# Kernel optimization log

Measured on AMD Instinct MI355X. Metric: run time of the kernel, lower is better.

Reference implementation:

```python
import jax, jax.numpy as jnp
import numpy as np

RADIUS = 2.0  # ball-query radius (float forward arg in the original; fixed here)


def _conv1x1(x, W, b):
    # 1x1 Conv2D over NHWC == per-point linear layer
    return jnp.einsum('bmsc,cd->bmsd', x, W) + b


def _ball_query(xyz, new_xyz, radius, nsample):
    """For each cluster center, take the first (by index) nsample points within
    radius, padding with the first found neighbor (TF ball-query semantics).
    xyz: (B,N,3), new_xyz: (B,M,3) -> idx (B,M,nsample) int32."""
    N = xyz.shape[1]
    d2 = jnp.sum((new_xyz[:, :, None, :] - xyz[:, None, :, :]) ** 2, axis=-1)  # (B,M,N)
    valid = d2 < radius * radius
    key = jnp.where(valid, jnp.arange(N, dtype=jnp.int32)[None, None, :], N)
    order = jnp.argsort(key, axis=-1)[..., :nsample]          # (B,M,nsample)
    skey = jnp.take_along_axis(key, order, axis=-1)
    idx = jnp.where(skey < N, order, order[..., :1])          # pad with first neighbor
    return idx


def setup_inputs() -> dict:
    key = jax.random.key(0)
    ks = jax.random.split(key, 8)
    B, N = 8, 8192
    xyz = jax.random.normal(ks[0], (B, N, 3), dtype=jnp.float32)

    def w(k, cin, cout):
        return (jax.random.normal(k, (cin, cout), dtype=jnp.float32) / np.sqrt(cin)).astype(jnp.float32)

    z = lambda c: jnp.zeros((c,), jnp.float32)
    inp = {
        'xyz': xyz,
        'W1': w(ks[1], 3, 64),    'b1': z(64),
        'W2': w(ks[2], 64, 128),  'b2': z(128),
        'W3': w(ks[3], 128, 256), 'b3': z(256),
        'W4': w(ks[4], 256, 128), 'b4': z(128),
        'W5': w(ks[5], 128, 64),  'b5': z(64),
        'Wa': w(ks[6], 64, 1),    'ba': z(1),
        'Wo': w(ks[7], 64, 2),    'bo': z(2),
        'num_clusters': 512,
        'num_samples': 64,
    }
    return inp


def reference(xyz, W1, b1, W2, b2, W3, b3, W4, b4, W5, b5, Wa, ba, Wo, bo,
              num_clusters, num_samples):
    # sample cluster centers (deterministic stand-in for random subsampling)
    new_xyz = xyz[:, :num_clusters]                                    # (B,M,3)
    idx = _ball_query(xyz, new_xyz, RADIUS, num_samples)               # (B,M,S)
    grouped = jax.vmap(lambda pts, i: pts[i])(xyz, idx)                # (B,M,S,3)
    g = (grouped - new_xyz[:, :, None, :]) / RADIUS                    # normalize_radius

    # shared per-point MLP (1x1 convs, relu)
    h = jax.nn.relu(_conv1x1(g, W1, b1))
    h = jax.nn.relu(_conv1x1(h, W2, b2))
    h = jax.nn.relu(_conv1x1(h, W3, b3))
    # MaxPoolAxis: max over samples, keepdims
    h = jnp.max(h, axis=2, keepdims=True)                              # (B,M,1,256)
    # mlp2 convs (linear, no activation in source)
    h = _conv1x1(h, W4, b4)
    h = _conv1x1(h, W5, b5)                                            # (B,M,1,64)

    attention = jax.nn.softplus(_conv1x1(h, Wa, ba))[:, :, 0, 0]       # (B,M)
    o = _conv1x1(h, Wo, bo)[:, :, 0, :]                                # (B,M,2)
    o = o / jnp.sqrt(jnp.maximum(jnp.sum(o * o, axis=-1, keepdims=True), 1e-8))
    orientation = jnp.arctan2(o[..., 1], o[..., 0])                    # (B,M)
    return new_xyz, idx, attention, orientation
```

## Files before the change

kernel.cpp:

```cpp
#include <hip/hip_runtime.h>
#include <math.h>

#define BB 8
#define NN 8192
#define MM 512
#define SS 64
#define NCLUST (BB*MM)

#define OUT_IDX   (BB*MM*3)
#define OUT_ATT   (OUT_IDX + BB*MM*SS)
#define OUT_ORI   (OUT_ATT + BB*MM)

#define WS_W3 8192

typedef short v8s __attribute__((ext_vector_type(8)));
typedef float v4f __attribute__((ext_vector_type(4)));

static __device__ __forceinline__ unsigned short f2bf(float x) {
    unsigned int u = __float_as_uint(x);
    u += 0x7FFFu + ((u >> 16) & 1u);
    return (unsigned short)(u >> 16);
}

__global__ void pack_weights(const float* __restrict__ W2,
                             const float* __restrict__ W3,
                             unsigned short* __restrict__ ws)
{
    const int gid = blockIdx.x * 256 + threadIdx.x;
    const float* W; unsigned short* dst; int N, kt, nt, lane;
    if (gid < 1024) {
        W = W2; N = 128;
        const int tile = gid >> 6; lane = gid & 63;
        kt = tile >> 3; nt = tile & 7;
        dst = ws + (size_t)(tile * 64 + lane) * 8;
    } else {
        const int g = gid - 1024;
        W = W3; N = 256;
        const int tile = g >> 6; lane = g & 63;
        kt = tile >> 4; nt = tile & 15;
        dst = ws + WS_W3 + (size_t)(tile * 64 + lane) * 8;
    }
    const int k0 = kt * 32 + (lane >> 4) * 8;
    const int n  = nt * 16 + (lane & 15);
    union { unsigned short u[8]; v8s v; } f;
    #pragma unroll
    for (int j = 0; j < 8; ++j) f.u[j] = f2bf(W[(k0 + j) * N + n]);
    *(v8s*)dst = f.v;
}

__global__ __launch_bounds__(256, 4) void feat3d_fused(
    const float* __restrict__ xyz,
    const float* __restrict__ W1, const float* __restrict__ b1,
    const float* __restrict__ b2, const float* __restrict__ b3,
    const unsigned short* __restrict__ Wp,
    const float* __restrict__ W4, const float* __restrict__ b4,
    const float* __restrict__ W5, const float* __restrict__ b5,
    const float* __restrict__ Wa, const float* __restrict__ ba,
    const float* __restrict__ Wo, const float* __restrict__ bo,
    float* __restrict__ out)
{
    __shared__ __align__(16) unsigned char lds[24576];
    unsigned short* a2p = (unsigned short*)lds;
    unsigned short* a3p = (unsigned short*)(lds + 8192);
    int*   ws_idx = (int*)(lds + 8192);
    float* ws_g   = (float*)(lds + 9216);
    int*   ls_cnt = (int*)(lds + 12288);
    float* ls_w1  = (float*)(lds + 12304);
    float* ls_g   = (float*)(lds + 13328);

    float* vbuf   = (float*)lds;
    float* h4part = (float*)(lds + 1024);
    float* h4f    = (float*)(lds + 5120);
    float* h5p    = (float*)(lds + 5632);

    const int t   = threadIdx.x;
    const int wv  = t >> 6;
    const int l   = t & 63;
    const int q   = l >> 4;
    const int r16 = l & 15;
    const int blk = blockIdx.x;
    const int b   = blk >> 9;
    const int m   = blk & 511;
    const float* xb = xyz + (size_t)b * (NN * 3);

    const v8s* W2f = (const v8s*)Wp;
    v8s bfr[2][2];
    #pragma unroll
    for (int kt = 0; kt < 2; ++kt)
        #pragma unroll
        for (int ni = 0; ni < 2; ++ni)
            bfr[kt][ni] = W2f[(kt*8 + 2*wv + ni)*64 + l];

    const float cx = xb[m*3+0], cy = xb[m*3+1], cz = xb[m*3+2];

    if (t < 3) out[(b*MM + m)*3 + t] = xb[m*3 + t];

    if (t < 64) {
        ls_w1[t*4+0] = W1[t];
        ls_w1[t*4+1] = W1[64 + t];
        ls_w1[t*4+2] = W1[128 + t];
        ls_w1[t*4+3] = b1[t];
    }

    {
        const int base = wv * 2048;
        int cntw = 0;
        for (int it = 0; it < 32 && cntw < SS; ++it) {
            const int j = base + it*64 + l;
            const float dx = xb[j*3+0] - cx;
            const float dy = xb[j*3+1] - cy;
            const float dz = xb[j*3+2] - cz;
            const float d2 = __fadd_rn(__fadd_rn(__fmul_rn(dx,dx), __fmul_rn(dy,dy)),
                                       __fmul_rn(dz,dz));
            const bool valid = d2 < 4.0f;
            const unsigned long long mask = __ballot(valid);
            const int below = __popcll(mask & ((1ull << l) - 1ull));
            const int pos = cntw + below;
            if (valid && pos < SS) {
                ws_idx[wv*64 + pos]      = j;
                ws_g[(wv*64 + pos)*3 + 0] = dx * 0.5f;
                ws_g[(wv*64 + pos)*3 + 1] = dy * 0.5f;
                ws_g[(wv*64 + pos)*3 + 2] = dz * 0.5f;
            }
            cntw += (int)__popcll(mask);
        }
        if (l == 0) ls_cnt[wv] = (cntw < SS) ? cntw : SS;
    }
    __syncthreads();

    if (t < SS) {
        const int c0 = ls_cnt[0], c1 = ls_cnt[1], c2 = ls_cnt[2], c3 = ls_cnt[3];
        int s, off;
        if (t < c0 + c1 + c2 + c3) {
            if (t < c0)                 { s = 0; off = t; }
            else if (t < c0 + c1)       { s = 1; off = t - c0; }
            else if (t < c0 + c1 + c2)  { s = 2; off = t - c0 - c1; }
            else                        { s = 3; off = t - c0 - c1 - c2; }
        } else {
            s = (c0 > 0) ? 0 : (c1 > 0) ? 1 : (c2 > 0) ? 2 : 3;
            off = 0;
        }
        const int e = s*64 + off;
        out[OUT_IDX + (b*MM + m)*SS + t] = (float)ws_idx[e];
        ls_g[t*4+0] = ws_g[e*3+0];
        ls_g[t*4+1] = ws_g[e*3+1];
        ls_g[t*4+2] = ws_g[e*3+2];
    }
    __syncthreads();

    {
        const int s = wv*16 + r16;
        const float4 g4 = *(const float4*)&ls_g[s*4];
        #pragma unroll
        for (int kt = 0; kt < 2; ++kt) {
            union { unsigned short u[8]; v8s v; } fr;
            #pragma unroll
            for (int j = 0; j < 8; ++j) {
                const int c = kt*32 + q*8 + j;
                const float4 w = *(const float4*)&ls_w1[c*4];
                const float h = fmaf(g4.x, w.x, fmaf(g4.y, w.y, fmaf(g4.z, w.z, w.w)));
                fr.u[j] = f2bf(fmaxf(h, 0.f));
            }
            *(v8s*)&a2p[((kt*4 + wv)*64 + l)*8] = fr.v;
        }
    }
    __syncthreads();

    {
        const v4f z = {0.f, 0.f, 0.f, 0.f};
        v4f acc[4][2];
        #pragma unroll
        for (int mt = 0; mt < 4; ++mt) { acc[mt][0] = z; acc[mt][1] = z; }

        #pragma unroll
        for (int kt = 0; kt < 2; ++kt)
            #pragma unroll
            for (int mt = 0; mt < 4; ++mt) {
                const v8s a = *(const v8s*)&a2p[((kt*4 + mt)*64 + l)*8];
                #pragma unroll
                for (int ni = 0; ni < 2; ++ni)
                    acc[mt][ni] = __builtin_amdgcn_mfma_f32_16x16x32_bf16(
                        a, bfr[kt][ni], acc[mt][ni], 0, 0, 0);
            }

        #pragma unroll
        for (int ni = 0; ni < 2; ++ni) {
            const int c2  = (2*wv + ni)*16 + r16;
            const float bias = b2[c2];
            const int kt3 = c2 >> 5;
            const int lhi = ((c2 >> 3) & 3) << 4;
            const int j3  = c2 & 7;
            #pragma unroll
            for (int mt = 0; mt < 4; ++mt)
                #pragma unroll
                for (int rg = 0; rg < 4; ++rg) {
                    const float h = fmaxf(acc[mt][ni][rg] + bias, 0.f);
                    const int s15 = q*4 + rg;
                    a3p[((kt3*4 + mt)*64 + (lhi | s15))*8 + j3] = f2bf(h);
                }
        }
    }
    __syncthreads();

    {
        const v8s* W3f = (const v8s*)(Wp + WS_W3);

        #pragma unroll
        for (int np = 0; np < 2; ++np) {
            const int nt0 = 4*wv + 2*np;
            const v4f z = {0.f, 0.f, 0.f, 0.f};
            v4f acc[4][2];
            #pragma unroll
            for (int mt = 0; mt < 4; ++mt) { acc[mt][0] = z; acc[mt][1] = z; }

            v8s bb0 = W3f[(0*16 + nt0    )*64 + l];
            v8s bb1 = W3f[(0*16 + nt0 + 1)*64 + l];
            #pragma unroll
            for (int kt = 0; kt < 4; ++kt) {
                v8s a[4];
                #pragma unroll
                for (int mt = 0; mt < 4; ++mt)
                    a[mt] = *(const v8s*)&a3p[((kt*4 + mt)*64 + l)*8];
                v8s nb0, nb1;
                if (kt < 3) {
                    nb0 = W3f[((kt+1)*16 + nt0    )*64 + l];
                    nb1 = W3f[((kt+1)*16 + nt0 + 1)*64 + l];
                }
                #pragma unroll
                for (int mt = 0; mt < 4; ++mt) {
                    acc[mt][0] = __builtin_amdgcn_mfma_f32_16x16x32_bf16(
                        a[mt], bb0, acc[mt][0], 0, 0, 0);
                    acc[mt][1] = __builtin_amdgcn_mfma_f32_16x16x32_bf16(
                        a[mt], bb1, acc[mt][1], 0, 0, 0);
                }
                if (kt < 3) { bb0 = nb0; bb1 = nb1; }
            }

            #pragma unroll
            for (int ni = 0; ni < 2; ++ni) {
                float mx = acc[0][ni][0];
                #pragma unroll
                for (int mt = 0; mt < 4; ++mt)
                    #pragma unroll
                    for (int rg = 0; rg < 4; ++rg)
                        mx = fmaxf(mx, acc[mt][ni][rg]);
                mx = fmaxf(mx, __shfl_xor(mx, 16));
                mx = fmaxf(mx, __shfl_xor(mx, 32));
                if (q == 0) {
                    const int c = (nt0 + ni)*16 + r16;
                    vbuf[c] = fmaxf(mx + b3[c], 0.f);
                }
            }
        }
    }
    __syncthreads();

    {
        const int cgp = t & 31;
        const int kp  = t >> 5;
        const float4* W4v = (const float4*)W4;
        const float4* vb4 = (const float4*)&vbuf[kp*32];
        float4 acc = make_float4(0.f, 0.f, 0.f, 0.f);
        #pragma unroll
        for (int kk4 = 0; kk4 < 8; ++kk4) {
            const float4 vv = vb4[kk4];
            const int k = kp*32 + kk4*4;
            const float4 w0 = W4v[(k+0)*32 + cgp];
            const float4 w1 = W4v[(k+1)*32 + cgp];
            const float4 w2 = W4v[(k+2)*32 + cgp];
            const float4 w3 = W4v[(k+3)*32 + cgp];
            acc.x = fmaf(vv.x, w0.x, fmaf(vv.y, w1.x, fmaf(vv.z, w2.x, fmaf(vv.w, w3.x, acc.x))));
            acc.y = fmaf(vv.x, w0.y, fmaf(vv.y, w1.y, fmaf(vv.z, w2.y, fmaf(vv.w, w3.y, acc.y))));
            acc.z = fmaf(vv.x, w0.z, fmaf(vv.y, w1.z, fmaf(vv.z, w2.z, fmaf(vv.w, w3.z, acc.z))));
            acc.w = fmaf(vv.x, w0.w, fmaf(vv.y, w1.w, fmaf(vv.z, w2.w, fmaf(vv.w, w3.w, acc.w))));
        }
        *(float4*)&h4part[kp*128 + cgp*4] = acc;
    }
    __syncthreads();
    if (t < 128) {
        float s = b4[t];
        #pragma unroll
        for (int kp = 0; kp < 8; ++kp) s += h4part[kp*128 + t];
        h4f[t] = s;
    }
    __syncthreads();

    {
        const int c5 = t & 63;
        const int kq = t >> 6;
        const float* W5c = W5 + c5;
        float acc = 0.f;
        for (int k = kq*32; k < kq*32 + 32; k += 4) {
            const float4 hh = *(const float4*)&h4f[k];
            acc = fmaf(hh.x, W5c[(k+0)*64],
                  fmaf(hh.y, W5c[(k+1)*64],
                  fmaf(hh.z, W5c[(k+2)*64],
                  fmaf(hh.w, W5c[(k+3)*64], acc))));
        }
        h5p[t] = acc;
    }
    __syncthreads();

    if (t < 64) {
        const float h5v = h5p[t] + h5p[64 + t] + h5p[128 + t] + h5p[192 + t] + b5[t];
        float va = h5v * Wa[t];
        float v0 = h5v * Wo[2*t + 0];
        float v1 = h5v * Wo[2*t + 1];
        #pragma unroll
        for (int off = 32; off > 0; off >>= 1) {
            va += __shfl_down(va, off);
            v0 += __shfl_down(v0, off);
            v1 += __shfl_down(v1, off);
        }
        if (t == 0) {
            const float a = va + ba[0];
            out[OUT_ATT + blk] = fmaxf(a, 0.f) + log1pf(expf(-fabsf(a)));
            out[OUT_ORI + blk] = atan2f(v1 + bo[1], v0 + bo[0]);
        }
    }
}

extern "C" void kernel_launch(void* const* d_in, const int* in_sizes, int n_in,
                              void* d_out, int out_size, void* d_ws, size_t ws_size,
                              hipStream_t stream) {
    const float* xyz = (const float*)d_in[0];
    const float* W1  = (const float*)d_in[1];
    const float* b1  = (const float*)d_in[2];
    const float* W2  = (const float*)d_in[3];
    const float* b2  = (const float*)d_in[4];
    const float* W3  = (const float*)d_in[5];
    const float* b3  = (const float*)d_in[6];
    const float* W4  = (const float*)d_in[7];
    const float* b4  = (const float*)d_in[8];
    const float* W5  = (const float*)d_in[9];
    const float* b5  = (const float*)d_in[10];
    const float* Wa  = (const float*)d_in[11];
    const float* ba  = (const float*)d_in[12];
    const float* Wo  = (const float*)d_in[13];
    const float* bo  = (const float*)d_in[14];

    unsigned short* ws = (unsigned short*)d_ws;

    pack_weights<<<dim3(20), dim3(256), 0, stream>>>(W2, W3, ws);
    feat3d_fused<<<dim3(NCLUST), dim3(256), 0, stream>>>(
        xyz, W1, b1, b2, b3, ws, W4, b4, W5, b5, Wa, ba, Wo, bo, (float*)d_out);
}
```

Before: 142.2 us.

## Process two clusters per 512-thread block with block-wide ordered ball query scan

Each block now handles two cluster centers with 512 threads, four waves per cluster. The ball query no longer gives each wave a fixed 2048-point slice. Instead it scans 256 points per step in order across four waves, shares ballot masks through LDS with a barrier each step, and stops once both clusters have 64 neighbors. This removes the over-scan of each wave's whole slice and amortizes weight loads across two clusters. The cost is a __syncthreads per 256 points, doubled LDS, and wave divergence when one cluster finishes early.

```diff
diff --git a/kernel.cpp b/kernel.cpp
--- a/kernel.cpp
+++ b/kernel.cpp
@@ -48,7 +48,7 @@
     *(v8s*)dst = f.v;
 }
 
-__global__ __launch_bounds__(256, 4) void feat3d_fused(
+__global__ __launch_bounds__(512, 4) void feat3d_fused(
     const float* __restrict__ xyz,
     const float* __restrict__ W1, const float* __restrict__ b1,
     const float* __restrict__ b2, const float* __restrict__ b3,
@@ -59,41 +59,42 @@
     const float* __restrict__ Wo, const float* __restrict__ bo,
     float* __restrict__ out)
 {
-    __shared__ __align__(16) unsigned char lds[24576];
+    __shared__ __align__(16) unsigned char lds[49152];
     unsigned short* a2p = (unsigned short*)lds;
-    unsigned short* a3p = (unsigned short*)(lds + 8192);
-    int*   ws_idx = (int*)(lds + 8192);
-    float* ws_g   = (float*)(lds + 9216);
-    int*   ls_cnt = (int*)(lds + 12288);
-    float* ls_w1  = (float*)(lds + 12304);
-    float* ls_g   = (float*)(lds + 13328);
+    unsigned short* a3p = (unsigned short*)(lds + 16384);
+    float* ls_w1  = (float*)(lds + 16384);
+    float* ls_g   = (float*)(lds + 17408);
+    int*   ls_idx = (int*)(lds + 19456);
+    unsigned long long* ls_mask = (unsigned long long*)(lds + 19968);
 
     float* vbuf   = (float*)lds;
-    float* h4part = (float*)(lds + 1024);
-    float* h4f    = (float*)(lds + 5120);
-    float* h5p    = (float*)(lds + 5632);
+    float* h4part = (float*)(lds + 2048);
+    float* h4f    = (float*)(lds + 10240);
+    float* h5p    = (float*)(lds + 11264);
 
     const int t   = threadIdx.x;
     const int wv  = t >> 6;
     const int l   = t & 63;
     const int q   = l >> 4;
     const int r16 = l & 15;
+    const int g   = wv >> 2;
+    const int wg  = wv & 3;
     const int blk = blockIdx.x;
-    const int b   = blk >> 9;
-    const int m   = blk & 511;
+    const int b   = blk >> 8;
+    const int m0  = (blk & 255) * 2;
     const float* xb = xyz + (size_t)b * (NN * 3);
 
     const v8s* W2f = (const v8s*)Wp;
-    v8s bfr[2][2];
-    #pragma unroll
-    for (int kt = 0; kt < 2; ++kt)
-        #pragma unroll
-        for (int ni = 0; ni < 2; ++ni)
-            bfr[kt][ni] = W2f[(kt*8 + 2*wv + ni)*64 + l];
-
-    const float cx = xb[m*3+0], cy = xb[m*3+1], cz = xb[m*3+2];
-
-    if (t < 3) out[(b*MM + m)*3 + t] = xb[m*3 + t];
+    const v8s bfr0 = W2f[(0*8 + wv)*64 + l];
+    const v8s bfr1 = W2f[(1*8 + wv)*64 + l];
+
+    const int mg = m0 + g;
+    const float cx = xb[mg*3+0], cy = xb[mg*3+1], cz = xb[mg*3+2];
+
+    if (t < 6) {
+        const int cl = t / 3, d = t - cl*3;
+        out[(b*MM + m0 + cl)*3 + d] = xb[(m0 + cl)*3 + d];
+    }
 
     if (t < 64) {
         ls_w1[t*4+0] = W1[t];
@@ -102,55 +103,73 @@
         ls_w1[t*4+3] = b1[t];
     }
 
-    {
-        const int base = wv * 2048;
-        int cntw = 0;
-        for (int it = 0; it < 32 && cntw < SS; ++it) {
-            const int j = base + it*64 + l;
-            const float dx = xb[j*3+0] - cx;
-            const float dy = xb[j*3+1] - cy;
-            const float dz = xb[j*3+2] - cz;
-            const float d2 = __fadd_rn(__fadd_rn(__fmul_rn(dx,dx), __fmul_rn(dy,dy)),
-                                       __fmul_rn(dz,dz));
-            const bool valid = d2 < 4.0f;
+    int cntA = 0, cntB = 0;
+    {
+        int base = 0, pb = 0;
+        while (base < NN && (cntA < SS || cntB < SS)) {
+            const int myCnt = g ? cntB : cntA;
+            int j = 0; float dx = 0.f, dy = 0.f, dz = 0.f; bool valid = false;
+            if (myCnt < SS) {
+                j = base + wg*64 + l;
+                dx = xb[j*3+0] - cx;
+                dy = xb[j*3+1] - cy;
+                dz = xb[j*3+2] - cz;
+                const float d2 = __fadd_rn(__fadd_rn(__fmul_rn(dx,dx), __fmul_rn(dy,dy)),
+                                           __fmul_rn(dz,dz));
+                valid = d2 < 4.0f;
+            }
             const unsigned long long mask = __ballot(valid);
-            const int below = __popcll(mask & ((1ull << l) - 1ull));
-            const int pos = cntw + below;
+            if (l == 0) ls_mask[pb*8 + wv] = mask;
+            __syncthreads();
+            const unsigned long long k0 = ls_mask[pb*8+0], k1 = ls_mask[pb*8+1],
+                                     k2 = ls_mask[pb*8+2], k3 = ls_mask[pb*8+3],
+                                     k4 = ls_mask[pb*8+4], k5 = ls_mask[pb*8+5],
+                                     k6 = ls_mask[pb*8+6], k7 = ls_mask[pb*8+7];
+            int below = __popcll(mask & ((1ull << l) - 1ull));
+            if (g == 0) {
+                if (wg > 0) below += (int)__popcll(k0);
+                if (wg > 1) below += (int)__popcll(k1);
+                if (wg > 2) below += (int)__popcll(k2);
+            } else {
+                if (wg > 0) below += (int)__popcll(k4);
+                if (wg > 1) below += (int)__popcll(k5);
+                if (wg > 2) below += (int)__popcll(k6);
+            }
+            const int pos = myCnt + below;
             if (valid && pos < SS) {
-                ws_idx[wv*64 + pos]      = j;
-                ws_g[(wv*64 + pos)*3 + 0] = dx * 0.5f;
-                ws_g[(wv*64 + pos)*3 + 1] = dy * 0.5f;
-                ws_g[(wv*64 + pos)*3 + 2] = dz * 0.5f;
-            }
-            cntw += (int)__popcll(mask);
-        }
-        if (l == 0) ls_cnt[wv] = (cntw < SS) ? cntw : SS;
-    }
-    __syncthreads();
-
-    if (t < SS) {
-        const int c0 = ls_cnt[0], c1 = ls_cnt[1], c2 = ls_cnt[2], c3 = ls_cnt[3];
-        int s, off;
-        if (t < c0 + c1 + c2 + c3) {
-            if (t < c0)                 { s = 0; off = t; }
-            else if (t < c0 + c1)       { s = 1; off = t - c0; }
-            else if (t < c0 + c1 + c2)  { s = 2; off = t - c0 - c1; }
-            else                        { s = 3; off = t - c0 - c1 - c2; }
-        } else {
-            s = (c0 > 0) ? 0 : (c1 > 0) ? 1 : (c2 > 0) ? 2 : 3;
-            off = 0;
-        }
-        const int e = s*64 + off;
-        out[OUT_IDX + (b*MM + m)*SS + t] = (float)ws_idx[e];
-        ls_g[t*4+0] = ws_g[e*3+0];
-        ls_g[t*4+1] = ws_g[e*3+1];
-        ls_g[t*4+2] = ws_g[e*3+2];
-    }
-    __syncthreads();
-
-    {
-        const int s = wv*16 + r16;
-        const float4 g4 = *(const float4*)&ls_g[s*4];
+                ls_idx[g*64 + pos]        = j;
+                ls_g[(g*64 + pos)*4 + 0]  = dx * 0.5f;
+                ls_g[(g*64 + pos)*4 + 1]  = dy * 0.5f;
+                ls_g[(g*64 + pos)*4 + 2]  = dz * 0.5f;
+            }
+            cntA += (int)(__popcll(k0) + __popcll(k1) + __popcll(k2) + __popcll(k3));
+            if (cntA > SS) cntA = SS;
+            cntB += (int)(__popcll(k4) + __popcll(k5) + __popcll(k6) + __popcll(k7));
+            if (cntB > SS) cntB = SS;
+            base += 256;
+            pb ^= 1;
+        }
+    }
+    __syncthreads();
+    if (t < 128) {
+        const int cl = t >> 6, s = t & 63;
+        const int cnt = cl ? cntB : cntA;
+        if (s >= cnt) {
+            ls_idx[cl*64 + s]       = ls_idx[cl*64];
+            ls_g[(cl*64 + s)*4 + 0] = ls_g[(cl*64)*4 + 0];
+            ls_g[(cl*64 + s)*4 + 1] = ls_g[(cl*64)*4 + 1];
+            ls_g[(cl*64 + s)*4 + 2] = ls_g[(cl*64)*4 + 2];
+        }
+    }
+    __syncthreads();
+    if (t < 128) {
+        const int cl = t >> 6, s = t & 63;
+        out[OUT_IDX + (b*MM + m0 + cl)*SS + s] = (float)ls_idx[cl*64 + s];
+    }
+
+    {
+        const int S = wv*16 + r16;
+        const float4 g4 = *(const float4*)&ls_g[S*4];
         #pragma unroll
         for (int kt = 0; kt < 2; ++kt) {
             union { unsigned short u[8]; v8s v; } fr;
@@ -161,53 +180,49 @@
                 const float h = fmaf(g4.x, w.x, fmaf(g4.y, w.y, fmaf(g4.z, w.z, w.w)));
                 fr.u[j] = f2bf(fmaxf(h, 0.f));
             }
-            *(v8s*)&a2p[((kt*4 + wv)*64 + l)*8] = fr.v;
+            *(v8s*)&a2p[((kt*8 + wv)*64 + l)*8] = fr.v;
         }
     }
     __syncthreads();
 
     {
         const v4f z = {0.f, 0.f, 0.f, 0.f};
-        v4f acc[4][2];
-        #pragma unroll
-        for (int mt = 0; mt < 4; ++mt) { acc[mt][0] = z; acc[mt][1] = z; }
-
-        #pragma unroll
-        for (int kt = 0; kt < 2; ++kt)
-            #pragma unroll
-            for (int mt = 0; mt < 4; ++mt) {
-                const v8s a = *(const v8s*)&a2p[((kt*4 + mt)*64 + l)*8];
-                #pragma unroll
-                for (int ni = 0; ni < 2; ++ni)
-                    acc[mt][ni] = __builtin_amdgcn_mfma_f32_16x16x32_bf16(
-                        a, bfr[kt][ni], acc[mt][ni], 0, 0, 0);
-            }
-
-        #pragma unroll
-        for (int ni = 0; ni < 2; ++ni) {
-            const int c2  = (2*wv + ni)*16 + r16;
-            const float bias = b2[c2];
-            const int kt3 = c2 >> 5;
-            const int lhi = ((c2 >> 3) & 3) << 4;
-            const int j3  = c2 & 7;
-            #pragma unroll
-            for (int mt = 0; mt < 4; ++mt)
-                #pragma unroll
-                for (int rg = 0; rg < 4; ++rg) {
-                    const float h = fmaxf(acc[mt][ni][rg] + bias, 0.f);
-                    const int s15 = q*4 + rg;
-                    a3p[((kt3*4 + mt)*64 + (lhi | s15))*8 + j3] = f2bf(h);
-                }
-        }
+        v4f acc[8];
+        #pragma unroll
+        for (int mt = 0; mt < 8; ++mt) acc[mt] = z;
+
+        #pragma unroll
+        for (int mt = 0; mt < 8; ++mt) {
+            const v8s a0 = *(const v8s*)&a2p[((0*8 + mt)*64 + l)*8];
+            acc[mt] = __builtin_amdgcn_mfma_f32_16x16x32_bf16(a0, bfr0, acc[mt], 0, 0, 0);
+            const v8s a1 = *(const v8s*)&a2p[((1*8 + mt)*64 + l)*8];
+            acc[mt] = __builtin_amdgcn_mfma_f32_16x16x32_bf16(a1, bfr1, acc[mt], 0, 0, 0);
+        }
+
+        const int c2  = wv*16 + r16;
+        const float bias = b2[c2];
+        const int kt3 = c2 >> 5;
+        const int lhi = ((c2 >> 3) & 3) << 4;
+        const int j3  = c2 & 7;
+        #pragma unroll
+        for (int mt = 0; mt < 8; ++mt)
+            #pragma unroll
+            for (int rg = 0; rg < 4; ++rg) {
+                const float h = fmaxf(acc[mt][rg] + bias, 0.f);
+                const int s15 = q*4 + rg;
+                a3p[((kt3*8 + mt)*64 + (lhi | s15))*8 + j3] = f2bf(h);
+            }
     }
     __syncthreads();
 
     {
         const v8s* W3f = (const v8s*)(Wp + WS_W3);
+        const int mh = wv >> 2;
+        const int nq = wv & 3;
 
         #pragma unroll
         for (int np = 0; np < 2; ++np) {
-            const int nt0 = 4*wv + 2*np;
+            const int nt0 = nq*4 + 2*np;
             const v4f z = {0.f, 0.f, 0.f, 0.f};
             v4f acc[4][2];
             #pragma unroll
@@ -220,7 +235,7 @@
                 v8s a[4];
                 #pragma unroll
                 for (int mt = 0; mt < 4; ++mt)
-                    a[mt] = *(const v8s*)&a3p[((kt*4 + mt)*64 + l)*8];
+                    a[mt] = *(const v8s*)&a3p[((kt*8 + mh*4 + mt)*64 + l)*8];
                 v8s nb0, nb1;
                 if (kt < 3) {
                     nb0 = W3f[((kt+1)*16 + nt0    )*64 + l];
@@ -248,7 +263,7 @@
                 mx = fmaxf(mx, __shfl_xor(mx, 32));
                 if (q == 0) {
                     const int c = (nt0 + ni)*16 + r16;
-                    vbuf[c] = fmaxf(mx + b3[c], 0.f);
+                    vbuf[mh*256 + c] = fmaxf(mx + b3[c], 0.f);
                 }
             }
         }
@@ -256,10 +271,12 @@
     __syncthreads();
 
     {
-        const int cgp = t & 31;
-        const int kp  = t >> 5;
+        const int cl  = t >> 8;
+        const int tt  = t & 255;
+        const int cgp = tt & 31;
+        const int kp  = tt >> 5;
         const float4* W4v = (const float4*)W4;
-        const float4* vb4 = (const float4*)&vbuf[kp*32];
+        const float4* vb4 = (const float4*)&vbuf[cl*256 + kp*32];
         float4 acc = make_float4(0.f, 0.f, 0.f, 0.f);
         #pragma unroll
         for (int kk4 = 0; kk4 < 8; ++kk4) {
@@ -274,48 +291,56 @@
             acc.z = fmaf(vv.x, w0.z, fmaf(vv.y, w1.z, fmaf(vv.z, w2.z, fmaf(vv.w, w3.z, acc.z))));
             acc.w = fmaf(vv.x, w0.w, fmaf(vv.y, w1.w, fmaf(vv.z, w2.w, fmaf(vv.w, w3.w, acc.w))));
         }
-        *(float4*)&h4part[kp*128 + cgp*4] = acc;
-    }
-    __syncthreads();
-    if (t < 128) {
-        float s = b4[t];
-        #pragma unroll
-        for (int kp = 0; kp < 8; ++kp) s += h4part[kp*128 + t];
-        h4f[t] = s;
-    }
-    __syncthreads();
-
-    {
-        const int c5 = t & 63;
-        const int kq = t >> 6;
+        *(float4*)&h4part[((cl*8 + kp)*128) + cgp*4] = acc;
+    }
+    __syncthreads();
+    if (t < 256) {
+        const int cl = t >> 7, c = t & 127;
+        float s = b4[c];
+        #pragma unroll
+        for (int kp = 0; kp < 8; ++kp) s += h4part[(cl*8 + kp)*128 + c];
+        h4f[cl*128 + c] = s;
+    }
+    __syncthreads();
+
+    {
+        const int cl = t >> 8;
+        const int tt = t & 255;
+        const int c5 = tt & 63;
+        const int kq = tt >> 6;
         const float* W5c = W5 + c5;
+        const float* h4c = h4f + cl*128;
         float acc = 0.f;
         for (int k = kq*32; k < kq*32 + 32; k += 4) {
-            const float4 hh = *(const float4*)&h4f[k];
+            const float4 hh = *(const float4*)&h4c[k];
             acc = fmaf(hh.x, W5c[(k+0)*64],
                   fmaf(hh.y, W5c[(k+1)*64],
                   fmaf(hh.z, W5c[(k+2)*64],
                   fmaf(hh.w, W5c[(k+3)*64], acc))));
         }
-        h5p[t] = acc;
-    }
-    __syncthreads();
-
-    if (t < 64) {
-        const float h5v = h5p[t] + h5p[64 + t] + h5p[128 + t] + h5p[192 + t] + b5[t];
-        float va = h5v * Wa[t];
-        float v0 = h5v * Wo[2*t + 0];
-        float v1 = h5v * Wo[2*t + 1];
+        h5p[(cl*4 + kq)*64 + c5] = acc;
+    }
+    __syncthreads();
+
+    if (t < 128) {
+        const int cl = t >> 6, ll = t & 63;
+        float h5v = b5[ll];
+        #pragma unroll
+        for (int kq = 0; kq < 4; ++kq) h5v += h5p[(cl*4 + kq)*64 + ll];
+        float va = h5v * Wa[ll];
+        float v0 = h5v * Wo[2*ll + 0];
+        float v1 = h5v * Wo[2*ll + 1];
         #pragma unroll
         for (int off = 32; off > 0; off >>= 1) {
             va += __shfl_down(va, off);
             v0 += __shfl_down(v0, off);
             v1 += __shfl_down(v1, off);
         }
-        if (t == 0) {
+        if (ll == 0) {
+            const int cg = b*MM + m0 + cl;
             const float a = va + ba[0];
-            out[OUT_ATT + blk] = fmaxf(a, 0.f) + log1pf(expf(-fabsf(a)));
-            out[OUT_ORI + blk] = atan2f(v1 + bo[1], v0 + bo[0]);
+            out[OUT_ATT + cg] = fmaxf(a, 0.f) + log1pf(expf(-fabsf(a)));
+            out[OUT_ORI + cg] = atan2f(v1 + bo[1], v0 + bo[0]);
         }
     }
 }
@@ -342,6 +367,6 @@
     unsigned short* ws = (unsigned short*)d_ws;
 
     pack_weights<<<dim3(20), dim3(256), 0, stream>>>(W2, W3, ws);
-    feat3d_fused<<<dim3(NCLUST), dim3(256), 0, stream>>>(
+    feat3d_fused<<<dim3(NCLUST/2), dim3(512), 0, stream>>>(
         xyz, W1, b1, b2, b3, ws, W4, b4, W5, b5, Wa, ba, Wo, bo, (float*)d_out);
 }
```

Result: no change. 143.7 us (+1.1%).
